# Optimization experiments

Hardware: AMD Instinct MI355X
Metric: run time of the kernel (lower is better)

## Reference

```python
import jax, jax.numpy as jnp
import numpy as np

N, F, H, L, E, C = 50000, 256, 64, 8, 1600000, 40
ALPHA, THETA = 0.1, 0.5


def setup_inputs() -> dict:
    key = jax.random.key(0)
    ks = jax.random.split(key, 8)
    x = jax.random.normal(ks[0], (N, F), jnp.float32)
    edge_index = jax.random.randint(ks[1], (2, E), 0, N)
    edge_weight = jax.random.uniform(ks[2], (E,), jnp.float32)
    W0 = jax.random.normal(ks[3], (F, H), jnp.float32) / np.sqrt(F).astype(np.float32)
    b0 = jnp.zeros((H,), jnp.float32)
    Wl = jax.random.normal(ks[4], (L, H, H), jnp.float32) / np.sqrt(H).astype(np.float32)
    W2 = jax.random.normal(ks[5], (H * H, C), jnp.float32) / np.sqrt(H * H).astype(np.float32)
    b2 = jnp.zeros((C,), jnp.float32)
    return dict(x=x, edge_index=edge_index, edge_weight=edge_weight,
                W0=W0, b0=b0, Wl=Wl, W2=W2, b2=b2)


def reference(x, edge_index, edge_weight, W0, b0, Wl, W2, b2):
    src, dst = edge_index[0], edge_index[1]
    # initial projection (dropout p=0.0 is identity)
    h0 = jax.nn.relu(x @ W0 + b0)          # [N, H]
    h = h0
    for l in range(L):
        # GCN2Conv, shared_weights=True, normalize=False
        # SpMM: agg[dst] += w * h[src]
        agg = jax.ops.segment_sum(edge_weight[:, None] * h[src], dst, num_segments=N)
        beta = jnp.float32(np.log(THETA / (l + 1) + 1.0))
        hmix = (1.0 - ALPHA) * agg + ALPHA * h0  # initial residual blend
        h = jax.nn.relu((1.0 - beta) * hmix + beta * (hmix @ Wl[l]))
    # outer-product head: [N,H,H] -> [N, H*H]
    op = jnp.einsum('ni,nj->nij', h, h).reshape(N, H * H)
    logits = op @ W2 + b2                  # [N, C]
    return jax.nn.log_softmax(logits, axis=-1)
```

## Files before the change

kernel.cpp:

```cpp
#include <hip/hip_runtime.h>
#include <hip/hip_bf16.h>
#include <math.h>

#define NN 50000
#define FF 256
#define HH 64
#define LL 8
#define EE 1600000
#define CC 40

#define BK 64
#define NB ((NN + BK - 1) / BK)
#define PBK 4096
#define NPART ((EE + PBK - 1) / PBK)

using short8 = __attribute__((ext_vector_type(8))) short;
using short4v = __attribute__((ext_vector_type(4))) short;
using f32x4  = __attribute__((ext_vector_type(4))) float;

static __device__ __forceinline__ unsigned short f2b(float f) {
    union { __hip_bfloat16 h; unsigned short u; } cv;
    cv.h = __float2bfloat16(f);
    return cv.u;
}
static __device__ __forceinline__ float b2f(unsigned short u) {
    return __uint_as_float((unsigned)u << 16);
}

__global__ void k_bhist(const int* __restrict__ dst, int* __restrict__ bcnt) {
    __shared__ int lh[NB];
    int t = threadIdx.x;
    int e0 = blockIdx.x * PBK;
    int e1 = min(e0 + PBK, EE);
    for (int i = t; i < NB; i += 256) lh[i] = 0;
    __syncthreads();
    for (int e = e0 + t; e < e1; e += 256)
        atomicAdd(&lh[(unsigned)dst[e] >> 6], 1);
    __syncthreads();
    for (int i = t; i < NB; i += 256)
        if (lh[i]) atomicAdd(&bcnt[i], lh[i]);
}

__global__ void k_bscan(const int* __restrict__ bcnt, int* __restrict__ bbase) {
    __shared__ int buf[1024];
    int t = threadIdx.x;
    int v = (t < NB) ? bcnt[t] : 0;
    int vin = v;
    buf[t] = v;
    __syncthreads();
    for (int off = 1; off < 1024; off <<= 1) {
        int u = (t >= off) ? buf[t - off] : 0;
        __syncthreads();
        buf[t] += u;
        __syncthreads();
    }
    if (t < NB) bbase[t] = buf[t] - vin;
    if (t == 0) bbase[NB] = EE;
}

__global__ void k_binit(const int* __restrict__ bbase, int* __restrict__ bcur) {
    int t = blockIdx.x * 256 + threadIdx.x;
    if (t < NB) bcur[t] = bbase[t];
}

__global__ void k_part(const int* __restrict__ src, const int* __restrict__ dst,
                       const float* __restrict__ w, int* __restrict__ bcur,
                       uint2* __restrict__ ebuk) {
    __shared__ int lh[NB];
    __shared__ int lbase[NB];
    int t = threadIdx.x;
    int e0 = blockIdx.x * PBK;
    int e1 = min(e0 + PBK, EE);
    for (int i = t; i < NB; i += 256) lh[i] = 0;
    __syncthreads();
    for (int e = e0 + t; e < e1; e += 256)
        atomicAdd(&lh[(unsigned)dst[e] >> 6], 1);
    __syncthreads();
    for (int i = t; i < NB; i += 256) {
        int c = lh[i];
        lbase[i] = c ? atomicAdd(&bcur[i], c) : 0;
    }
    __syncthreads();
    for (int i = t; i < NB; i += 256) lh[i] = 0;
    __syncthreads();
    for (int e = e0 + t; e < e1; e += 256) {
        int d = dst[e];
        int b = (unsigned)d >> 6;
        int r = atomicAdd(&lh[b], 1);
        ebuk[lbase[b] + r] = make_uint2(((unsigned)src[e] << 16) | (unsigned)f2b(w[e]),
                                        (unsigned)d);
    }
}

__global__ void k_sub(const int* __restrict__ bbase, const uint2* __restrict__ ebuk,
                      unsigned* __restrict__ pay, int* __restrict__ row_ptr) {
    __shared__ int lcnt[BK];
    __shared__ int lcur[BK];
    int b = blockIdx.x;
    int d0 = b * BK;
    int bksz = min(BK, NN - d0);
    int t = threadIdx.x;
    if (t < BK) lcnt[t] = 0;
    __syncthreads();
    int lo = bbase[b], hi = bbase[b + 1];
    for (int i = lo + t; i < hi; i += 256)
        atomicAdd(&lcnt[ebuk[i].y - d0], 1);
    __syncthreads();
    if (t < 64) {
        int vin = lcnt[t];
        int v = vin;
        for (int off = 1; off < 64; off <<= 1) {
            int u = __shfl_up(v, off);
            if (t >= off) v += u;
        }
        int excl = v - vin + lo;
        lcur[t] = excl;
        if (t < bksz) row_ptr[d0 + t] = excl;
    }
    if (b == NB - 1 && t == 0) row_ptr[NN] = EE;
    __syncthreads();
    for (int i = lo + t; i < hi; i += 256) {
        uint2 pk = ebuk[i];
        int p = atomicAdd(&lcur[pk.y - d0], 1);
        pay[p] = pk.x;
    }
}

__global__ void k_w2b(const float* __restrict__ W2, unsigned short* __restrict__ W2b) {
    int o = blockIdx.x * 256 + threadIdx.x;
    if (o < 3 * 64 * 16 * 64) {
        int j = o & 63;
        int cr = (o >> 6) & 15;
        int i = (o >> 10) & 63;
        int ct = o >> 16;
        int c = ct * 16 + cr;
        float v = (c < CC) ? W2[((size_t)i * 64 + j) * CC + c] : 0.f;
        W2b[o] = f2b(v);
    }
}

__global__ __launch_bounds__(512) void k_h0m(const float* __restrict__ x,
                                             const float* __restrict__ W0,
                                             const float* __restrict__ b0,
                                             float* __restrict__ h0f,
                                             unsigned short* __restrict__ h0b) {
    __shared__ __align__(16) __hip_bfloat16 ax[256][72];
    __shared__ __align__(16) __hip_bfloat16 bw[64][72];

    int tid = threadIdx.x;
    int lane = tid & 63;
    int w = tid >> 6;
    int nbase = blockIdx.x * 256;

    f32x4 acc[2][4];
#pragma unroll
    for (int nf = 0; nf < 2; ++nf)
#pragma unroll
        for (int cf = 0; cf < 4; ++cf) acc[nf][cf] = (f32x4){0.f, 0.f, 0.f, 0.f};

    int arow = w * 32 + (lane & 15);
    int kq = (lane >> 4) * 8;

    for (int kc = 0; kc < 4; ++kc) {
        __syncthreads();
#pragma unroll
        for (int p = 0; p < 8; ++p) {
            int q = p * 512 + tid;
            int r = q >> 4, cq = q & 15;
            int node = nbase + r;
            float4 v = {0.f, 0.f, 0.f, 0.f};
            if (node < NN) v = *(const float4*)&x[(size_t)node * FF + kc * 64 + cq * 4];
            __hip_bfloat16* d = &ax[r][cq * 4];
            d[0] = __float2bfloat16(v.x);
            d[1] = __float2bfloat16(v.y);
            d[2] = __float2bfloat16(v.z);
            d[3] = __float2bfloat16(v.w);
        }
#pragma unroll
        for (int u = 0; u < 8; ++u) {
            int k = (tid >> 6) * 8 + u;
            float v = W0[(size_t)(kc * 64 + k) * HH + lane];
            bw[lane][k] = __float2bfloat16(v);
        }
        __syncthreads();
#pragma unroll
        for (int ks = 0; ks < 2; ++ks) {
            short8 a0 = *(const short8*)&ax[arow][ks * 32 + kq];
            short8 a1 = *(const short8*)&ax[arow + 16][ks * 32 + kq];
#pragma unroll
            for (int cf = 0; cf < 4; ++cf) {
                short8 b = *(const short8*)&bw[cf * 16 + (lane & 15)][ks * 32 + kq];
                acc[0][cf] = __builtin_amdgcn_mfma_f32_16x16x32_bf16(a0, b, acc[0][cf], 0, 0, 0);
                acc[1][cf] = __builtin_amdgcn_mfma_f32_16x16x32_bf16(a1, b, acc[1][cf], 0, 0, 0);
            }
        }
    }

#pragma unroll
    for (int nf = 0; nf < 2; ++nf) {
#pragma unroll
        for (int cf = 0; cf < 4; ++cf) {
            int c = cf * 16 + (lane & 15);
            float bias = b0[c];
#pragma unroll
            for (int r = 0; r < 4; ++r) {
                int node = nbase + w * 32 + nf * 16 + ((lane >> 4) << 2) + r;
                if (node < NN) {
                    float v = fmaxf(acc[nf][cf][r] + bias, 0.f);
                    h0f[(size_t)node * HH + c] = v;
                    h0b[(size_t)node * HH + c] = f2b(v);
                }
            }
        }
    }
}

__global__ __launch_bounds__(256, 8) void k_layer(
        const unsigned short* __restrict__ hin, const float* __restrict__ h0,
        const int* __restrict__ row_ptr, const unsigned* __restrict__ pay,
        const float* __restrict__ Wl, float beta,
        unsigned short* __restrict__ hout) {
    int lane = threadIdx.x & 63;
    int half = lane >> 5;
    int j = lane & 31;
    int n0 = (blockIdx.x * 4 + (threadIdx.x >> 6)) * 4;

    const unsigned* __restrict__ hin32 = (const unsigned*)hin;

    float hmix[4];
#pragma unroll
    for (int u = 0; u < 4; ++u) {
        int n = n0 + u;
        int rb = row_ptr[n], re = row_ptr[n + 1];
        float ax0 = 0.f, ay0 = 0.f, ax1 = 0.f, ay1 = 0.f;
        for (int base = rb; base < re; base += 64) {
            int idx = base + lane;
            unsigned pv = (idx < re) ? pay[idx] : 0u;
            int ecnt = min(64, re - base);
            for (int k = 0; k < ecnt; k += 8) {
                unsigned pk[8];
#pragma unroll
                for (int t = 0; t < 8; t++)
                    pk[t] = (unsigned)__builtin_amdgcn_readlane((int)pv, k + t);
                unsigned m0 = half ? pk[1] : pk[0];
                unsigned m1 = half ? pk[3] : pk[2];
                unsigned m2 = half ? pk[5] : pk[4];
                unsigned m3 = half ? pk[7] : pk[6];
                unsigned u0 = hin32[(size_t)(m0 >> 16) * 32 + j];
                unsigned u1 = hin32[(size_t)(m1 >> 16) * 32 + j];
                unsigned u2 = hin32[(size_t)(m2 >> 16) * 32 + j];
                unsigned u3 = hin32[(size_t)(m3 >> 16) * 32 + j];
                float w0 = __uint_as_float((m0 & 0xFFFFu) << 16);
                float w1 = __uint_as_float((m1 & 0xFFFFu) << 16);
                float w2 = __uint_as_float((m2 & 0xFFFFu) << 16);
                float w3 = __uint_as_float((m3 & 0xFFFFu) << 16);
                ax0 = fmaf(w0, __uint_as_float(u0 << 16), ax0);
                ay0 = fmaf(w0, __uint_as_float(u0 & 0xFFFF0000u), ay0);
                ax1 = fmaf(w1, __uint_as_float(u1 << 16), ax1);
                ay1 = fmaf(w1, __uint_as_float(u1 & 0xFFFF0000u), ay1);
                ax0 = fmaf(w2, __uint_as_float(u2 << 16), ax0);
                ay0 = fmaf(w2, __uint_as_float(u2 & 0xFFFF0000u), ay0);
                ax1 = fmaf(w3, __uint_as_float(u3 << 16), ax1);
                ay1 = fmaf(w3, __uint_as_float(u3 & 0xFFFF0000u), ay1);
            }
        }
        float ax = ax0 + ax1, ay = ay0 + ay1;
        ax += __shfl_xor(ax, 32);
        ay += __shfl_xor(ay, 32);
        float vx = __shfl(ax, lane >> 1);
        float vy = __shfl(ay, lane >> 1);
        float acc = (lane & 1) ? vy : vx;
        hmix[u] = fmaf(0.9f, acc, 0.1f * h0[(size_t)n * HH + lane]);
    }

    int hb[4];
#pragma unroll
    for (int u = 0; u < 4; ++u) hb[u] = __float_as_int(hmix[u]);
    float a2[4] = {0.f, 0.f, 0.f, 0.f};
#pragma unroll
    for (int jj = 0; jj < HH; jj++) {
        float wr = Wl[jj * HH + lane];
#pragma unroll
        for (int u = 0; u < 4; ++u) {
            float hj = __int_as_float(__builtin_amdgcn_readlane(hb[u], jj));
            a2[u] = fmaf(hj, wr, a2[u]);
        }
    }
#pragma unroll
    for (int u = 0; u < 4; ++u) {
        float outv = (1.f - beta) * hmix[u] + beta * a2[u];
        hout[(size_t)(n0 + u) * HH + lane] = f2b(fmaxf(outv, 0.f));
    }
}

__global__ __launch_bounds__(512) void k_head(const unsigned short* __restrict__ h,
                                              const unsigned short* __restrict__ W2b,
                                              const float* __restrict__ b2,
                                              float* __restrict__ out) {
    __shared__ __align__(16) unsigned short Bl[32 * 1056];

    int tid = threadIdx.x;
    int lane = tid & 63;
    int w = tid >> 6;
    int nbase = blockIdx.x * 256;
    int ct = blockIdx.y;
    int c0 = ct * 16;

    int kq = (lane >> 4) * 8;
    int arow = w * 32 + (lane & 15);
    int rb4 = w * 32 + ((lane >> 4) << 2);

    int ra0 = min(nbase + arow, NN - 1);
    int ra1 = min(nbase + arow + 16, NN - 1);
    short8 af00 = *(const short8*)&h[(size_t)ra0 * HH + kq];
    short8 af01 = *(const short8*)&h[(size_t)ra0 * HH + 32 + kq];
    short8 af10 = *(const short8*)&h[(size_t)ra1 * HH + kq];
    short8 af11 = *(const short8*)&h[(size_t)ra1 * HH + 32 + kq];

    const unsigned short* srow[8];
#pragma unroll
    for (int r = 0; r < 4; ++r) {
        srow[r]     = &h[(size_t)min(nbase + rb4 + r, NN - 1) * HH];
        srow[4 + r] = &h[(size_t)min(nbase + rb4 + 16 + r, NN - 1) * HH];
    }

    const f32x4 zf = (f32x4){0.f, 0.f, 0.f, 0.f};
    f32x4 acc0 = zf, acc1 = zf;

    const unsigned short* __restrict__ Wslice = W2b + (size_t)ct * 65536;

    for (int ph = 0; ph < 2; ++ph) {
        __syncthreads();
        const unsigned short* src = Wslice + (size_t)ph * 32768;
#pragma unroll
        for (int rnd = 0; rnd < 8; ++rnd) {
            int cid = rnd * 512 + tid;
            int il = cid >> 7;
            int rem = cid & 127;
            int cr = rem >> 3;
            int jg = rem & 7;
            *(short8*)&Bl[il * 1056 + cr * 66 + jg * 8] =
                *(const short8*)&src[(size_t)cid * 8];
        }
        __syncthreads();

#pragma unroll
        for (int ihl = 0; ihl < 8; ++ihl) {
            int ibase = ihl * 4;
            int ig = ph * 32 + ibase;
            short8 B00 = *(const short8*)&Bl[(ibase + 0) * 1056 + (lane & 15) * 66 + kq];
            short8 B01 = *(const short8*)&Bl[(ibase + 0) * 1056 + (lane & 15) * 66 + 32 + kq];
            short8 B10 = *(const short8*)&Bl[(ibase + 1) * 1056 + (lane & 15) * 66 + kq];
            short8 B11 = *(const short8*)&Bl[(ibase + 1) * 1056 + (lane & 15) * 66 + 32 + kq];
            short8 B20 = *(const short8*)&Bl[(ibase + 2) * 1056 + (lane & 15) * 66 + kq];
            short8 B21 = *(const short8*)&Bl[(ibase + 2) * 1056 + (lane & 15) * 66 + 32 + kq];
            short8 B30 = *(const short8*)&Bl[(ibase + 3) * 1056 + (lane & 15) * 66 + kq];
            short8 B31 = *(const short8*)&Bl[(ibase + 3) * 1056 + (lane & 15) * 66 + 32 + kq];
            short4v sa0 = *(const short4v*)&srow[0][ig];
            short4v sa1 = *(const short4v*)&srow[1][ig];
            short4v sa2 = *(const short4v*)&srow[2][ig];
            short4v sa3 = *(const short4v*)&srow[3][ig];
            short4v sb0 = *(const short4v*)&srow[4][ig];
            short4v sb1 = *(const short4v*)&srow[5][ig];
            short4v sb2 = *(const short4v*)&srow[6][ig];
            short4v sb3 = *(const short4v*)&srow[7][ig];

#define ILB(IL, B0, B1)                                                          \
            {                                                                    \
                f32x4 t;                                                         \
                t = __builtin_amdgcn_mfma_f32_16x16x32_bf16(af00, B0, zf, 0, 0, 0); \
                t = __builtin_amdgcn_mfma_f32_16x16x32_bf16(af01, B1, t, 0, 0, 0);  \
                acc0[0] = fmaf(b2f((unsigned short)sa0[IL]), t[0], acc0[0]);     \
                acc0[1] = fmaf(b2f((unsigned short)sa1[IL]), t[1], acc0[1]);     \
                acc0[2] = fmaf(b2f((unsigned short)sa2[IL]), t[2], acc0[2]);     \
                acc0[3] = fmaf(b2f((unsigned short)sa3[IL]), t[3], acc0[3]);     \
                t = __builtin_amdgcn_mfma_f32_16x16x32_bf16(af10, B0, zf, 0, 0, 0); \
                t = __builtin_amdgcn_mfma_f32_16x16x32_bf16(af11, B1, t, 0, 0, 0);  \
                acc1[0] = fmaf(b2f((unsigned short)sb0[IL]), t[0], acc1[0]);     \
                acc1[1] = fmaf(b2f((unsigned short)sb1[IL]), t[1], acc1[1]);     \
                acc1[2] = fmaf(b2f((unsigned short)sb2[IL]), t[2], acc1[2]);     \
                acc1[3] = fmaf(b2f((unsigned short)sb3[IL]), t[3], acc1[3]);     \
            }
            ILB(0, B00, B01)
            ILB(1, B10, B11)
            ILB(2, B20, B21)
            ILB(3, B30, B31)
#undef ILB
        }
    }

    int c = c0 + (lane & 15);
    if (c < CC) {
        float bias = b2[c];
#pragma unroll
        for (int r = 0; r < 4; ++r) {
            int node0 = nbase + rb4 + r;
            if (node0 < NN) out[(size_t)node0 * CC + c] = acc0[r] + bias;
            int node1 = nbase + rb4 + 16 + r;
            if (node1 < NN) out[(size_t)node1 * CC + c] = acc1[r] + bias;
        }
    }
}

__global__ void k_lsm(float* __restrict__ out) {
    int lane = threadIdx.x & 63;
    int n = (blockIdx.x * 256 + threadIdx.x) >> 6;
    if (n >= NN) return;
    float x = (lane < CC) ? out[(size_t)n * CC + lane] : -INFINITY;
    float m = x;
    for (int off = 32; off; off >>= 1) m = fmaxf(m, __shfl_xor(m, off));
    float e = (lane < CC) ? expf(x - m) : 0.f;
    float s = e;
    for (int off = 32; off; off >>= 1) s += __shfl_xor(s, off);
    float lse = m + logf(s);
    if (lane < CC) out[(size_t)n * CC + lane] = x - lse;
}

extern "C" void kernel_launch(void* const* d_in, const int* in_sizes, int n_in,
                              void* d_out, int out_size, void* d_ws, size_t ws_size,
                              hipStream_t stream) {
    const float* x  = (const float*)d_in[0];
    const int*   ei = (const int*)d_in[1];
    const float* ew = (const float*)d_in[2];
    const float* W0 = (const float*)d_in[3];
    const float* b0 = (const float*)d_in[4];
    const float* Wl = (const float*)d_in[5];
    const float* W2 = (const float*)d_in[6];
    const float* b2 = (const float*)d_in[7];
    float* out = (float*)d_out;

    char* ws = (char*)d_ws;
    size_t off = 0;
    auto alloc = [&](size_t b) { size_t o = off; off += (b + 255) & ~(size_t)255; return o; };
    float*          h0f = (float*)(ws + alloc((size_t)NN * HH * 4));
    unsigned short* h0b = (unsigned short*)(ws + alloc((size_t)NN * HH * 2));
    unsigned short* hA  = (unsigned short*)(ws + alloc((size_t)NN * HH * 2));
    unsigned short* hB  = (unsigned short*)(ws + alloc((size_t)NN * HH * 2));
    int*      bcnt    = (int*)(ws + alloc((size_t)NB * 4));
    int*      bbase   = (int*)(ws + alloc((size_t)(NB + 1) * 4));
    int*      bcur    = (int*)(ws + alloc((size_t)NB * 4));
    int*      row_ptr = (int*)(ws + alloc((size_t)(NN + 1) * 4));
    uint2*    ebuk    = (uint2*)(ws + alloc((size_t)EE * 8));
    unsigned* pay     = (unsigned*)(ws + alloc((size_t)EE * 4));
    unsigned short* W2b = (unsigned short*)(ws + alloc((size_t)3 * 64 * 16 * 64 * 2));

    const int* srcp = ei;
    const int* dstp = ei + EE;

    hipMemsetAsync(bcnt, 0, (size_t)NB * 4, stream);
    k_bhist<<<NPART, 256, 0, stream>>>(dstp, bcnt);
    k_bscan<<<1, 1024, 0, stream>>>(bcnt, bbase);
    k_binit<<<(NB + 255) / 256, 256, 0, stream>>>(bbase, bcur);
    k_part<<<NPART, 256, 0, stream>>>(srcp, dstp, ew, bcur, ebuk);
    k_sub<<<NB, 256, 0, stream>>>(bbase, ebuk, pay, row_ptr);
    k_w2b<<<768, 256, 0, stream>>>(W2, W2b);

    k_h0m<<<196, 512, 0, stream>>>(x, W0, b0, h0f, h0b);

    const unsigned short* hin = h0b;
    unsigned short* ho = hA;
    for (int l = 0; l < LL; l++) {
        float beta = (float)log(0.5 / (double)(l + 1) + 1.0);
        k_layer<<<3125, 256, 0, stream>>>(hin, h0f, row_ptr, pay,
                                          Wl + (size_t)l * HH * HH, beta, ho);
        hin = ho;
        ho = (ho == hA) ? hB : hA;
    }

    k_head<<<dim3(196, 3), 512, 0, stream>>>(hin, W2b, b2, out);
    k_lsm<<<(NN * 64 + 255) / 256, 256, 0, stream>>>(out);
}
```

Before: 476.2 us.

## Split SpMM by source-node half into two passes for cache locality

Each node's edge list is partitioned by whether the source index is below 25000. Every layer then runs two kernels: the first gathers from the low half of node features and writes a float partial sum to a buffer, and the second gathers from the high half, adds the partial, and applies the mixing and the weight matrix. The goal is to shrink each pass's gather working set so it fits in cache better. In exchange it adds an extra kernel launch per layer, writes and reads a 12.8 MB fp32 buffer, and makes the CSR build do extra atomics.

```diff
diff --git a/kernel.cpp b/kernel.cpp
--- a/kernel.cpp
+++ b/kernel.cpp
@@ -8,6 +8,7 @@
 #define LL 8
 #define EE 1600000
 #define CC 40
+#define CHS 25000
 
 #define BK 64
 #define NB ((NN + BK - 1) / BK)
@@ -93,18 +94,25 @@
 }
 
 __global__ void k_sub(const int* __restrict__ bbase, const uint2* __restrict__ ebuk,
-                      unsigned* __restrict__ pay, int* __restrict__ row_ptr) {
+                      unsigned* __restrict__ pay, int* __restrict__ row_ptr,
+                      int* __restrict__ row_mid) {
     __shared__ int lcnt[BK];
-    __shared__ int lcur[BK];
+    __shared__ int lcnt0[BK];
+    __shared__ int lcur0[BK];
+    __shared__ int lcur1[BK];
     int b = blockIdx.x;
     int d0 = b * BK;
     int bksz = min(BK, NN - d0);
     int t = threadIdx.x;
-    if (t < BK) lcnt[t] = 0;
+    if (t < BK) { lcnt[t] = 0; lcnt0[t] = 0; }
     __syncthreads();
     int lo = bbase[b], hi = bbase[b + 1];
-    for (int i = lo + t; i < hi; i += 256)
-        atomicAdd(&lcnt[ebuk[i].y - d0], 1);
+    for (int i = lo + t; i < hi; i += 256) {
+        uint2 pk = ebuk[i];
+        int dl = pk.y - d0;
+        atomicAdd(&lcnt[dl], 1);
+        if ((pk.x >> 16) < CHS) atomicAdd(&lcnt0[dl], 1);
+    }
     __syncthreads();
     if (t < 64) {
         int vin = lcnt[t];
@@ -113,15 +121,21 @@
             int u = __shfl_up(v, off);
             if (t >= off) v += u;
         }
-        int excl = v - vin + lo;
-        lcur[t] = excl;
-        if (t < bksz) row_ptr[d0 + t] = excl;
+        int start = v - vin + lo;
+        lcur0[t] = start;
+        lcur1[t] = start + lcnt0[t];
+        if (t < bksz) {
+            row_ptr[d0 + t] = start;
+            row_mid[d0 + t] = start + lcnt0[t];
+        }
     }
     if (b == NB - 1 && t == 0) row_ptr[NN] = EE;
     __syncthreads();
     for (int i = lo + t; i < hi; i += 256) {
         uint2 pk = ebuk[i];
-        int p = atomicAdd(&lcur[pk.y - d0], 1);
+        int dl = pk.y - d0;
+        int p = ((pk.x >> 16) < CHS) ? atomicAdd(&lcur0[dl], 1)
+                                     : atomicAdd(&lcur1[dl], 1);
         pay[p] = pk.x;
     }
 }
@@ -215,11 +229,10 @@
     }
 }
 
-__global__ __launch_bounds__(256, 8) void k_layer(
-        const unsigned short* __restrict__ hin, const float* __restrict__ h0,
-        const int* __restrict__ row_ptr, const unsigned* __restrict__ pay,
-        const float* __restrict__ Wl, float beta,
-        unsigned short* __restrict__ hout) {
+__global__ __launch_bounds__(256, 8) void k_layer_p0(
+        const unsigned short* __restrict__ hin,
+        const int* __restrict__ row_ptr, const int* __restrict__ row_mid,
+        const unsigned* __restrict__ pay, float* __restrict__ accbuf) {
     int lane = threadIdx.x & 63;
     int half = lane >> 5;
     int j = lane & 31;
@@ -227,11 +240,10 @@
 
     const unsigned* __restrict__ hin32 = (const unsigned*)hin;
 
-    float hmix[4];
 #pragma unroll
     for (int u = 0; u < 4; ++u) {
         int n = n0 + u;
-        int rb = row_ptr[n], re = row_ptr[n + 1];
+        int rb = row_ptr[n], re = row_mid[n];
         float ax0 = 0.f, ay0 = 0.f, ax1 = 0.f, ay1 = 0.f;
         for (int base = rb; base < re; base += 64) {
             int idx = base + lane;
@@ -269,7 +281,68 @@
         ay += __shfl_xor(ay, 32);
         float vx = __shfl(ax, lane >> 1);
         float vy = __shfl(ay, lane >> 1);
-        float acc = (lane & 1) ? vy : vx;
+        float accv = (lane & 1) ? vy : vx;
+        accbuf[(size_t)n * HH + lane] = accv;
+    }
+}
+
+__global__ __launch_bounds__(256, 8) void k_layer_p1(
+        const unsigned short* __restrict__ hin, const float* __restrict__ h0,
+        const int* __restrict__ row_ptr, const int* __restrict__ row_mid,
+        const unsigned* __restrict__ pay, const float* __restrict__ accbuf,
+        const float* __restrict__ Wl, float beta,
+        unsigned short* __restrict__ hout) {
+    int lane = threadIdx.x & 63;
+    int half = lane >> 5;
+    int j = lane & 31;
+    int n0 = (blockIdx.x * 4 + (threadIdx.x >> 6)) * 4;
+
+    const unsigned* __restrict__ hin32 = (const unsigned*)hin;
+
+    float hmix[4];
+#pragma unroll
+    for (int u = 0; u < 4; ++u) {
+        int n = n0 + u;
+        int rb = row_mid[n], re = row_ptr[n + 1];
+        float ax0 = 0.f, ay0 = 0.f, ax1 = 0.f, ay1 = 0.f;
+        for (int base = rb; base < re; base += 64) {
+            int idx = base + lane;
+            unsigned pv = (idx < re) ? pay[idx] : 0u;
+            int ecnt = min(64, re - base);
+            for (int k = 0; k < ecnt; k += 8) {
+                unsigned pk[8];
+#pragma unroll
+                for (int t = 0; t < 8; t++)
+                    pk[t] = (unsigned)__builtin_amdgcn_readlane((int)pv, k + t);
+                unsigned m0 = half ? pk[1] : pk[0];
+                unsigned m1 = half ? pk[3] : pk[2];
+                unsigned m2 = half ? pk[5] : pk[4];
+                unsigned m3 = half ? pk[7] : pk[6];
+                unsigned u0 = hin32[(size_t)(m0 >> 16) * 32 + j];
+                unsigned u1 = hin32[(size_t)(m1 >> 16) * 32 + j];
+                unsigned u2 = hin32[(size_t)(m2 >> 16) * 32 + j];
+                unsigned u3 = hin32[(size_t)(m3 >> 16) * 32 + j];
+                float w0 = __uint_as_float((m0 & 0xFFFFu) << 16);
+                float w1 = __uint_as_float((m1 & 0xFFFFu) << 16);
+                float w2 = __uint_as_float((m2 & 0xFFFFu) << 16);
+                float w3 = __uint_as_float((m3 & 0xFFFFu) << 16);
+                ax0 = fmaf(w0, __uint_as_float(u0 << 16), ax0);
+                ay0 = fmaf(w0, __uint_as_float(u0 & 0xFFFF0000u), ay0);
+                ax1 = fmaf(w1, __uint_as_float(u1 << 16), ax1);
+                ay1 = fmaf(w1, __uint_as_float(u1 & 0xFFFF0000u), ay1);
+                ax0 = fmaf(w2, __uint_as_float(u2 << 16), ax0);
+                ay0 = fmaf(w2, __uint_as_float(u2 & 0xFFFF0000u), ay0);
+                ax1 = fmaf(w3, __uint_as_float(u3 << 16), ax1);
+                ay1 = fmaf(w3, __uint_as_float(u3 & 0xFFFF0000u), ay1);
+            }
+        }
+        float ax = ax0 + ax1, ay = ay0 + ay1;
+        ax += __shfl_xor(ax, 32);
+        ay += __shfl_xor(ay, 32);
+        float vx = __shfl(ax, lane >> 1);
+        float vy = __shfl(ay, lane >> 1);
+        float accv = (lane & 1) ? vy : vx;
+        float acc = accv + accbuf[(size_t)n * HH + lane];
         hmix[u] = fmaf(0.9f, acc, 0.1f * h0[(size_t)n * HH + lane]);
     }
 
@@ -436,10 +509,12 @@
     unsigned short* h0b = (unsigned short*)(ws + alloc((size_t)NN * HH * 2));
     unsigned short* hA  = (unsigned short*)(ws + alloc((size_t)NN * HH * 2));
     unsigned short* hB  = (unsigned short*)(ws + alloc((size_t)NN * HH * 2));
+    float*    accbuf  = (float*)(ws + alloc((size_t)NN * HH * 4));
     int*      bcnt    = (int*)(ws + alloc((size_t)NB * 4));
     int*      bbase   = (int*)(ws + alloc((size_t)(NB + 1) * 4));
     int*      bcur    = (int*)(ws + alloc((size_t)NB * 4));
     int*      row_ptr = (int*)(ws + alloc((size_t)(NN + 1) * 4));
+    int*      row_mid = (int*)(ws + alloc((size_t)NN * 4));
     uint2*    ebuk    = (uint2*)(ws + alloc((size_t)EE * 8));
     unsigned* pay     = (unsigned*)(ws + alloc((size_t)EE * 4));
     unsigned short* W2b = (unsigned short*)(ws + alloc((size_t)3 * 64 * 16 * 64 * 2));
@@ -452,7 +527,7 @@
     k_bscan<<<1, 1024, 0, stream>>>(bcnt, bbase);
     k_binit<<<(NB + 255) / 256, 256, 0, stream>>>(bbase, bcur);
     k_part<<<NPART, 256, 0, stream>>>(srcp, dstp, ew, bcur, ebuk);
-    k_sub<<<NB, 256, 0, stream>>>(bbase, ebuk, pay, row_ptr);
+    k_sub<<<NB, 256, 0, stream>>>(bbase, ebuk, pay, row_ptr, row_mid);
     k_w2b<<<768, 256, 0, stream>>>(W2, W2b);
 
     k_h0m<<<196, 512, 0, stream>>>(x, W0, b0, h0f, h0b);
@@ -461,8 +536,9 @@
     unsigned short* ho = hA;
     for (int l = 0; l < LL; l++) {
         float beta = (float)log(0.5 / (double)(l + 1) + 1.0);
-        k_layer<<<3125, 256, 0, stream>>>(hin, h0f, row_ptr, pay,
-                                          Wl + (size_t)l * HH * HH, beta, ho);
+        k_layer_p0<<<3125, 256, 0, stream>>>(hin, row_ptr, row_mid, pay, accbuf);
+        k_layer_p1<<<3125, 256, 0, stream>>>(hin, h0f, row_ptr, row_mid, pay, accbuf,
+                                             Wl + (size_t)l * HH * HH, beta, ho);
         hin = ho;
         ho = (ho == hA) ? hB : hA;
     }
```

Measured after the change: 556.8 us. 16.9% more time.
